# Performance work log

Hardware: AMD Instinct MI355X
Metric: run time of the kernel (lower is better)

The kernel has to match this reference:

```python
import jax, jax.numpy as jnp
import numpy as np

ROPE_DIM = 16      # RotaryEmbedding(dim=16)
MAX_FREQ = 256.0   # freqs_for='pixel'
NUM_HEADS = 16


def _axis_freqs(n):
    # pixel mode: base freqs = linspace(1, max_freq/2, dim//2) * pi, pos = linspace(-1, 1, n)
    base = jnp.linspace(1.0, MAX_FREQ / 2.0, ROPE_DIM // 2) * jnp.pi  # (8,)
    pos = jnp.linspace(-1.0, 1.0, n)                                   # (n,)
    f = pos[:, None] * base[None, :]                                   # (n, 8)
    return jnp.repeat(f, 2, axis=-1)                                   # (n, 16) interleaved pairs


def axial_freqs(T, H, W):
    ft = jnp.broadcast_to(_axis_freqs(T)[:, None, None, :], (T, H, W, ROPE_DIM))
    fh = jnp.broadcast_to(_axis_freqs(H)[None, :, None, :], (T, H, W, ROPE_DIM))
    fw = jnp.broadcast_to(_axis_freqs(W)[None, None, :, :], (T, H, W, ROPE_DIM))
    return jnp.concatenate([ft, fh, fw], axis=-1)  # (T, H, W, 48)


def rotate_half(x):
    # interleaved pairs: (..., d*2) -> rotate each (x1, x2) -> (-x2, x1)
    x = x.reshape(*x.shape[:-1], -1, 2)
    x1, x2 = x[..., 0], x[..., 1]
    return jnp.stack([-x2, x1], axis=-1).reshape(*x.shape[:-2], -1)


def apply_rope(freqs, t):
    # freqs: (T, H, W, rot_dim); t: (B, nh, T, H, W, hd); rotate first rot_dim dims
    rd = freqs.shape[-1]
    tm, tr = t[..., :rd], t[..., rd:]
    tm = tm * jnp.cos(freqs) + rotate_half(tm) * jnp.sin(freqs)
    return jnp.concatenate([tm, tr], axis=-1)


def setup_inputs() -> dict:
    key = jax.random.key(0)
    k1, k2, k3, k4 = jax.random.split(key, 4)
    B, N, C = 2, 2048, 1152
    return {
        "x": jax.random.normal(k1, (B, N, C), dtype=jnp.float32),
        "Wqkv": jax.random.normal(k2, (C, 3 * C), dtype=jnp.float32) * 0.02,
        "Wproj": jax.random.normal(k3, (C, C), dtype=jnp.float32) * 0.02,
        "bproj": jax.random.normal(k4, (C,), dtype=jnp.float32) * 0.02,
        "T": 8, "H": 16, "W": 16,
    }


def reference(x, Wqkv, Wproj, bproj, T, H, W):
    B, N, C = x.shape
    nh = NUM_HEADS
    hd = C // nh
    qkv = (x @ Wqkv).reshape(B, N, 3, nh, hd).transpose(2, 0, 3, 1, 4)  # (3, B, nh, N, hd)
    q, k, v = qkv[0], qkv[1], qkv[2]
    # tokens -> video grid
    q = q.reshape(B, nh, T, H, W, hd)
    k = k.reshape(B, nh, T, H, W, hd)
    freqs = axial_freqs(T, H, W)  # (T, H, W, 48)
    q = apply_rope(freqs, q).reshape(B, nh, N, hd)
    k = apply_rope(freqs, k).reshape(B, nh, N, hd)
    # SDPA (no mask, no dropout in eval / kv_cache=None path)
    scale = 1.0 / np.sqrt(hd)
    attn = jax.nn.softmax(jnp.einsum('bhqd,bhkd->bhqk', q, k) * scale, axis=-1)
    o = jnp.einsum('bhqk,bhkd->bhqd', attn, v)  # (B, nh, N, hd)
    o = o.transpose(0, 2, 1, 3).reshape(B, N, C)
    return o @ Wproj + bproj
```

## Files before the change

kernel.cpp:

```cpp
#include <hip/hip_runtime.h>
#include <hip/hip_bf16.h>

#define B_   2
#define N_   2048
#define C_   1152
#define NH   16
#define HD   72
#define HDP  96
#define HDV  80
#define QSTR 3584
#define KROW 104
#define VROW 72
#define KVB  64
#define KCH  832
#define TCH  1552
#define WCH  388

typedef __attribute__((ext_vector_type(8))) short bf16x8;
typedef __attribute__((ext_vector_type(4))) float f32x4;

__device__ __forceinline__ short f2bf(float f) {
  union { float fv; unsigned int u; } v; v.fv = f;
  unsigned int r = v.u + 0x7fffu + ((v.u >> 16) & 1u);
  return (short)(r >> 16);
}

__device__ __forceinline__ float bf2f(short s) {
  union { unsigned u; float f; } v; v.u = ((unsigned)(unsigned short)s) << 16;
  return v.f;
}

__device__ __forceinline__ unsigned pack_bf16(float a, float b) {
  union { __hip_bfloat162 h; unsigned u; } c;
  c.h = __float22bfloat162_rn(make_float2(a, b));
  return c.u;
}

__device__ __forceinline__ void gload_lds16(const short* g, short* l) {
  __builtin_amdgcn_global_load_lds(
      (const __attribute__((address_space(1))) unsigned int*)g,
      (__attribute__((address_space(3))) unsigned int*)l, 16, 0, 0);
}

__global__ __launch_bounds__(256) void prep(
    const float* __restrict__ x, short* __restrict__ xb,
    const float* __restrict__ Wqkv, short* __restrict__ Wt,
    const float* __restrict__ Wproj, short* __restrict__ Wpt) {
  int bid = blockIdx.x;
  if (bid < 4608) {
    const int i = bid * 256 + threadIdx.x;
    float4 v = ((const float4*)x)[i];
    short4 s;
    s.x = f2bf(v.x); s.y = f2bf(v.y); s.z = f2bf(v.z); s.w = f2bf(v.w);
    ((short4*)xb)[i] = s;
    return;
  }
  bid -= 4608;
  const float* src; short* dst; int Cc, bx, by;
  if (bid < 4032) {
    bx = bid % 112; by = bid / 112; src = Wqkv; dst = Wt; Cc = 3456;
  } else {
    bid -= 4032;
    bx = bid % 36; by = bid / 36; src = Wproj; dst = Wpt; Cc = 1152;
  }
  __shared__ float tile[32][33];
  const int c0 = bx * 32, r0 = by * 32;
  const int tx = threadIdx.x & 31, ty = threadIdx.x >> 5;
  for (int i = ty; i < 32; i += 8)
    tile[i][tx] = (c0 + tx < Cc) ? src[(long)(r0 + i) * Cc + c0 + tx] : 0.f;
  __syncthreads();
  for (int i = ty; i < 32; i += 8)
    dst[(long)(c0 + i) * 1152 + r0 + tx] = f2bf(tile[tx][i]);
}

template<bool BIAS, bool OBF>
__global__ __launch_bounds__(256, 2) void gemm_bt(
    const short* __restrict__ A, const short* __restrict__ Bt,
    void* __restrict__ Cv, const float* __restrict__ bias,
    int M, int N, int K) {
  __shared__ __align__(16) short As[2][128 * 32];
  __shared__ __align__(16) short Bs[2][128 * 32];
  const int t = threadIdx.x;
  const int lane = t & 63, wid = t >> 6;
  const int fr = lane & 15, fq = lane >> 4;

  int lin = blockIdx.y * gridDim.x + blockIdx.x;
  const int q8 = (int)(gridDim.x * gridDim.y) >> 3;
  lin = (lin & 7) * q8 + (lin >> 3);
  const int bm = lin / (int)gridDim.x;
  const int bn = lin - bm * (int)gridDim.x;

  const int wr = (wid >> 1) * 64, wc = (wid & 1) * 64;

  const int srow = t >> 2;
  const int scol = (t & 3) * 8;
  const short* Ag = A + (long)(bm * 128 + srow) * K + scol;
  const short* Bg = Bt + (long)(bn * 128 + srow) * K + scol;

  f32x4 acc[4][4] = {};

  auto STAGE = [&](int kt, int bufi) {
    gload_lds16(Ag + kt * 32,                &As[bufi][t * 8]);
    gload_lds16(Ag + kt * 32 + (long)64 * K, &As[bufi][2048 + t * 8]);
    gload_lds16(Bg + kt * 32,                &Bs[bufi][t * 8]);
    gload_lds16(Bg + kt * 32 + (long)64 * K, &Bs[bufi][2048 + t * 8]);
  };

  const int NKT = K / 32;
  STAGE(0, 0);

  for (int kt = 0; kt < NKT; ++kt) {
    const int cur = kt & 1;
    if (kt + 1 < NKT) {
      STAGE(kt + 1, cur ^ 1);
      asm volatile("s_waitcnt vmcnt(4)" ::: "memory");
    } else {
      asm volatile("s_waitcnt vmcnt(0)" ::: "memory");
    }
    __builtin_amdgcn_s_barrier();

    bf16x8 af[4], bf[4];
    #pragma unroll
    for (int i = 0; i < 4; ++i)
      af[i] = *(const bf16x8*)(&As[cur][(wr + i * 16 + fr) * 32 + fq * 8]);
    #pragma unroll
    for (int j = 0; j < 4; ++j)
      bf[j] = *(const bf16x8*)(&Bs[cur][(wc + j * 16 + fr) * 32 + fq * 8]);
    __builtin_amdgcn_s_setprio(1);
    #pragma unroll
    for (int i = 0; i < 4; ++i)
      #pragma unroll
      for (int j = 0; j < 4; ++j)
        acc[i][j] = __builtin_amdgcn_mfma_f32_16x16x32_bf16(af[i], bf[j], acc[i][j], 0, 0, 0);
    __builtin_amdgcn_s_setprio(0);
    __builtin_amdgcn_s_barrier();
  }

  #pragma unroll
  for (int i = 0; i < 4; ++i) {
    #pragma unroll
    for (int j = 0; j < 4; ++j) {
      const long row0 = (long)bm * 128 + wr + i * 16 + fq * 4;
      const int col = bn * 128 + wc + j * 16 + fr;
      const float bv = BIAS ? bias[col] : 0.f;
      #pragma unroll
      for (int r = 0; r < 4; ++r) {
        const float val = acc[i][j][r] + bv;
        if constexpr (OBF)
          ((short*)Cv)[(row0 + r) * (long)N + col] = f2bf(val);
        else
          ((float*)Cv)[(row0 + r) * (long)N + col] = val;
      }
    }
  }
}

__global__ __launch_bounds__(512, 2) void gemm_bt256(
    const short* __restrict__ A, const short* __restrict__ Bt,
    short* __restrict__ Cv, int M, int N, int K) {
  __shared__ __align__(16) short As[2][256 * 64];
  __shared__ __align__(16) short Bs[2][256 * 64];
  const int t = threadIdx.x;
  const int lane = t & 63, wid = t >> 6;
  const int fr = lane & 15, fq = lane >> 4;
  const int wm = wid >> 2, wn = wid & 3;
  const int rx = fr & 7;

  int lin = blockIdx.y * gridDim.x + blockIdx.x;
  const int q8 = (int)(gridDim.x * gridDim.y) >> 3;
  lin = (lin & 7) * q8 + (lin >> 3);
  const int bm = lin / (int)gridDim.x;
  const int bn = lin - bm * (int)gridDim.x;

  int soff[4];
  #pragma unroll
  for (int r = 0; r < 4; ++r) {
    const int p = r * 512 + t;
    const int row = p >> 3, pc = p & 7;
    soff[r] = row * K + (pc ^ (row & 7)) * 8;
  }
  const short* Ag = A + (long)bm * 256 * K;
  const short* Bg = Bt + (long)bn * 256 * K;

  f32x4 acc[8][4] = {};

  const int NKT = K / 64;
  #pragma unroll
  for (int r = 0; r < 4; ++r)
    gload_lds16(Ag + soff[r], &As[0][(r * 512 + t) * 8]);
  #pragma unroll
  for (int r = 0; r < 4; ++r)
    gload_lds16(Bg + soff[r], &Bs[0][(r * 512 + t) * 8]);

  for (int kt = 0; kt < NKT; ++kt) {
    const int cur = kt & 1;
    const bool pre = (kt + 1 < NKT);
    asm volatile("s_waitcnt vmcnt(0)" ::: "memory");
    __builtin_amdgcn_s_barrier();
    const short* Ac = &As[cur][0];
    const short* Bc = &Bs[cur][0];
    bf16x8 af[4][2], bf0[2][2], bf1[2][2];

    if (pre) {
      #pragma unroll
      for (int r = 0; r < 4; ++r)
        gload_lds16(Ag + soff[r] + (kt + 1) * 64, &As[cur ^ 1][(r * 512 + t) * 8]);
    }
    #pragma unroll
    for (int i = 0; i < 4; ++i)
      #pragma unroll
      for (int kk = 0; kk < 2; ++kk)
        af[i][kk] = *(const bf16x8*)(Ac + (wm * 128 + i * 16 + fr) * 64 + (((kk * 4 + fq) ^ rx) * 8));
    #pragma unroll
    for (int j = 0; j < 2; ++j)
      #pragma unroll
      for (int kk = 0; kk < 2; ++kk)
        bf0[j][kk] = *(const bf16x8*)(Bc + (wn * 64 + j * 16 + fr) * 64 + (((kk * 4 + fq) ^ rx) * 8));
    __builtin_amdgcn_s_setprio(1);
    #pragma unroll
    for (int i = 0; i < 4; ++i)
      #pragma unroll
      for (int j = 0; j < 2; ++j)
        #pragma unroll
        for (int kk = 0; kk < 2; ++kk)
          acc[i][j] = __builtin_amdgcn_mfma_f32_16x16x32_bf16(af[i][kk], bf0[j][kk], acc[i][j], 0, 0, 0);
    __builtin_amdgcn_s_setprio(0);

    if (pre) {
      #pragma unroll
      for (int r = 0; r < 4; ++r)
        gload_lds16(Bg + soff[r] + (kt + 1) * 64, &Bs[cur ^ 1][(r * 512 + t) * 8]);
    }
    #pragma unroll
    for (int j = 0; j < 2; ++j)
      #pragma unroll
      for (int kk = 0; kk < 2; ++kk)
        bf1[j][kk] = *(const bf16x8*)(Bc + (wn * 64 + 32 + j * 16 + fr) * 64 + (((kk * 4 + fq) ^ rx) * 8));
    __builtin_amdgcn_s_setprio(1);
    #pragma unroll
    for (int i = 0; i < 4; ++i)
      #pragma unroll
      for (int j = 0; j < 2; ++j)
        #pragma unroll
        for (int kk = 0; kk < 2; ++kk)
          acc[i][2 + j] = __builtin_amdgcn_mfma_f32_16x16x32_bf16(af[i][kk], bf1[j][kk], acc[i][2 + j], 0, 0, 0);
    __builtin_amdgcn_s_setprio(0);

    #pragma unroll
    for (int i = 0; i < 4; ++i)
      #pragma unroll
      for (int kk = 0; kk < 2; ++kk)
        af[i][kk] = *(const bf16x8*)(Ac + (wm * 128 + 64 + i * 16 + fr) * 64 + (((kk * 4 + fq) ^ rx) * 8));
    __builtin_amdgcn_s_setprio(1);
    #pragma unroll
    for (int i = 0; i < 4; ++i)
      #pragma unroll
      for (int j = 0; j < 2; ++j)
        #pragma unroll
        for (int kk = 0; kk < 2; ++kk)
          acc[4 + i][j] = __builtin_amdgcn_mfma_f32_16x16x32_bf16(af[i][kk], bf0[j][kk], acc[4 + i][j], 0, 0, 0);
    __builtin_amdgcn_s_setprio(0);

    __builtin_amdgcn_s_setprio(1);
    #pragma unroll
    for (int i = 0; i < 4; ++i)
      #pragma unroll
      for (int j = 0; j < 2; ++j)
        #pragma unroll
        for (int kk = 0; kk < 2; ++kk)
          acc[4 + i][2 + j] = __builtin_amdgcn_mfma_f32_16x16x32_bf16(af[i][kk], bf1[j][kk], acc[4 + i][2 + j], 0, 0, 0);
    __builtin_amdgcn_s_setprio(0);
  }

  #pragma unroll
  for (int mi = 0; mi < 8; ++mi) {
    #pragma unroll
    for (int j = 0; j < 4; ++j) {
      const long row0 = (long)bm * 256 + wm * 128 + (mi >> 2) * 64 + (mi & 3) * 16 + fq * 4;
      const int col = bn * 256 + wn * 64 + j * 16 + fr;
      #pragma unroll
      for (int r = 0; r < 4; ++r)
        Cv[(row0 + r) * (long)N + col] = f2bf(acc[mi][j][r]);
    }
  }
}

__global__ __launch_bounds__(256) void rope_pack(
    const short* __restrict__ QKV, short* __restrict__ Qp,
    short* __restrict__ Kp, short* __restrict__ Vt) {
  const int blk = blockIdx.x;
  const int nt = blk & 15;
  const int h = (blk >> 4) & 15;
  const int b = blk >> 8;
  const int t = threadIdx.x;
  const int n0 = nt * 128;
  const float qscale = 0.17002324f;
  const float PI = 3.14159265358979323846f;
  const long bhn = ((long)(b * NH + h)) * N_;

  for (int idx = t; idx < 128 * 48; idx += 256) {
    const int r = idx / 48;
    const int p = idx - r * 48;
    const int n = n0 + r;
    float cs = 1.f, sn = 0.f;
    if (p < 24) {
      float pos;
      if (p < 8)       pos = -1.f + (2.f / 7.f)  * (float)(n >> 8);
      else if (p < 16) pos = -1.f + (2.f / 15.f) * (float)((n >> 4) & 15);
      else             pos = -1.f + (2.f / 15.f) * (float)(n & 15);
      const float base = (1.f + (127.f / 7.f) * (float)(p & 7)) * PI;
      const float f = pos * base;
      cs = cosf(f); sn = sinf(f);
    }
    const long rowbase = ((long)(b * N_ + n)) * QSTR + h * HD + 2 * p;
    {
      float vx = 0.f, vy = 0.f;
      if (p < 36) {
        short2 v2 = *(const short2*)(QKV + rowbase);
        vx = bf2f(v2.x); vy = bf2f(v2.y);
      }
      const float o0 = vx * cs - vy * sn;
      const float o1 = vy * cs + vx * sn;
      short2 ov; ov.x = f2bf(o0 * qscale); ov.y = f2bf(o1 * qscale);
      *(short2*)(Qp + (bhn + n) * HDP + 2 * p) = ov;
    }
    {
      float vx = 0.f, vy = 0.f;
      if (p < 36) {
        short2 v2 = *(const short2*)(QKV + rowbase + C_);
        vx = bf2f(v2.x); vy = bf2f(v2.y);
      }
      const float o0 = vx * cs - vy * sn;
      const float o1 = vy * cs + vx * sn;
      short2 ov; ov.x = f2bf(o0); ov.y = f2bf(o1);
      *(short2*)(Kp + (bhn + n) * HDP + 2 * p) = ov;
    }
  }

  __shared__ short vt[128][82];
  for (int idx = t; idx < 128 * 40; idx += 256) {
    const int r = idx / 40, p = idx - r * 40;
    short2 v2; v2.x = 0; v2.y = 0;
    if (p < 36)
      v2 = *(const short2*)(QKV + ((long)(b * N_ + n0 + r)) * QSTR + 2 * C_ + h * HD + 2 * p);
    *(short2*)(&vt[r][2 * p]) = v2;
  }
  __syncthreads();
  for (int idx = t; idx < HDV * 128; idx += 256) {
    const int d = idx >> 7, nn = idx & 127;
    const int c = nn & 31;
    const int nsrc = (nn & 96) | (((c >> 2) & 1) * 16 + ((c >> 3) & 3) * 4 + (c & 3));
    Vt[(((long)(b * NH + h)) * HDV + d) * N_ + n0 + nn] = vt[nsrc][d];
  }
}

#define QKT_STEP(BUFI, S)                                                      \
  {                                                                            \
    const short* KsC_ = &KV[(BUFI)][0];                                        \
    __builtin_amdgcn_s_setprio(1);                                             \
    _Pragma("unroll")                                                          \
    for (int j = 0; j < 4; ++j) {                                              \
      _Pragma("unroll")                                                        \
      for (int kk = 0; kk < 3; ++kk) {                                         \
        bf16x8 kf = *(const bf16x8*)(KsC_ + (j * 16 + fr) * KROW + (kk * 4 + fq) * 8); \
        S[0][j] = __builtin_amdgcn_mfma_f32_16x16x32_bf16(kf, qf[0][kk], S[0][j], 0, 0, 0); \
        S[1][j] = __builtin_amdgcn_mfma_f32_16x16x32_bf16(kf, qf[1][kk], S[1][j], 0, 0, 0); \
      }                                                                        \
    }                                                                          \
    __builtin_amdgcn_s_setprio(0);                                             \
  }

#define ATTN_STEP(T, SCUR, SNEXT)                                              \
  {                                                                            \
    const int t_ = (T);                                                        \
          \
    _Pragma("unroll")                                                          \
    for (int i = 0; i < 2; ++i) {                                              \
      float psum = 0.f;                                                        \
      _Pragma("unroll")                                                        \
      for (int j = 0; j < 4; ++j)                                              \
        _Pragma("unroll")                                                      \
        for (int r = 0; r < 4; ++r) {                                          \
          const float p = __builtin_amdgcn_exp2f(SCUR[i][j][r]);               \
          SCUR[i][j][r] = p;                                                   \
          psum += p;                                                           \
        }                                                                      \
      l_[i] += psum;                                                           \
    }                                                                          \
    asm volatile("s_waitcnt vmcnt(0)" ::: "memory");                           \
    __builtin_amdgcn_s_barrier();                                              \
    if (t_ + 2 < 32) STAGE(t_ + 2, (t_ + 2) % 3);                              \
    if (t_ + 1 < 32) {                                                         \
      _Pragma("unroll")                                                        \
      for (int i = 0; i < 2; ++i)                                              \
        _Pragma("unroll")                                                      \
        for (int j = 0; j < 4; ++j)                                            \
          SNEXT[i][j] = (f32x4){0.f, 0.f, 0.f, 0.f};                           \
      QKT_STEP((t_ + 1) % 3, SNEXT);                                           \
    }                                                                          \
                    \
    const short* VsC_ = &KV[t_ % 3][KCH * 8];                                  \
    __builtin_amdgcn_s_setprio(1);                                             \
    _Pragma("unroll")                                                          \
    for (int g = 0; g < 2; ++g) {                                              \
      union { unsigned u[4]; bf16x8 v; } pf0, pf1;                             \
      pf0.u[0] = pack_bf16(SCUR[0][2 * g][0],     SCUR[0][2 * g][1]);          \
      pf0.u[1] = pack_bf16(SCUR[0][2 * g][2],     SCUR[0][2 * g][3]);          \
      pf0.u[2] = pack_bf16(SCUR[0][2 * g + 1][0], SCUR[0][2 * g + 1][1]);      \
      pf0.u[3] = pack_bf16(SCUR[0][2 * g + 1][2], SCUR[0][2 * g + 1][3]);      \
      pf1.u[0] = pack_bf16(SCUR[1][2 * g][0],     SCUR[1][2 * g][1]);          \
      pf1.u[1] = pack_bf16(SCUR[1][2 * g][2],     SCUR[1][2 * g][3]);          \
      pf1.u[2] = pack_bf16(SCUR[1][2 * g + 1][0], SCUR[1][2 * g + 1][1]);      \
      pf1.u[3] = pack_bf16(SCUR[1][2 * g + 1][2], SCUR[1][2 * g + 1][3]);      \
      _Pragma("unroll")                                                        \
      for (int jd = 0; jd < 5; ++jd) {                                         \
        bf16x8 vf = *(const bf16x8*)(VsC_ + (jd * 16 + fr) * VROW + (g * 4 + fq) * 8); \
        accO[0][jd] = __builtin_amdgcn_mfma_f32_16x16x32_bf16(pf0.v, vf, accO[0][jd], 0, 0, 0); \
        accO[1][jd] = __builtin_amdgcn_mfma_f32_16x16x32_bf16(pf1.v, vf, accO[1][jd], 0, 0, 0); \
      }                                                                        \
    }                                                                          \
    __builtin_amdgcn_s_setprio(0);                                             \
  }

__global__ __launch_bounds__(256, 2) void attn(
    const short* __restrict__ Qp, const short* __restrict__ Kp,
    const short* __restrict__ Vt, short* __restrict__ Aproj) {
  __shared__ __align__(16) short KV[3][TCH * 8];
  int blk = blockIdx.x;
  blk = (blk & 7) * 64 + (blk >> 3);
  const int qt = blk & 15;
  const int h = (blk >> 4) & 15;
  const int b = blk >> 8;
  const int t = threadIdx.x, lane = t & 63, wid = t >> 6;
  const int fr = lane & 15, fq = lane >> 4;

  const long bh = (long)(b * NH + h);
  const short* Qg = Qp + (bh * N_ + qt * 128) * HDP;
  const short* Kg = Kp + bh * N_ * HDP;
  const short* Vg = Vt + bh * HDV * N_;

  const short* sb[7];
  int sstr[7];
  #pragma unroll
  for (int it = 0; it < 7; ++it) {
    int g = wid * WCH + (it < 6 ? it * 64 + lane : 384 + lane);
    if (g >= TCH) g = TCH - 1;
    if (g < KCH) {
      const int r = g / 13, c = g - r * 13;
      sb[it] = Kg + r * HDP + (c < 12 ? c * 8 : 0);
      sstr[it] = KVB * HDP;
    } else {
      const int v = g - KCH;
      const int r = v / 9, c = v - r * 9;
      sb[it] = Vg + r * N_ + (c < 8 ? c * 8 : 0);
      sstr[it] = KVB;
    }
  }

  bf16x8 qf[2][3];
  #pragma unroll
  for (int i = 0; i < 2; ++i)
    #pragma unroll
    for (int kk = 0; kk < 3; ++kk)
      qf[i][kk] = *(const bf16x8*)(Qg + (wid * 32 + i * 16 + fr) * HDP + kk * 32 + fq * 8);

  f32x4 accO[2][5] = {};
  float l_[2] = {0.f, 0.f};

  auto STAGE = [&](int kt, int bufi) {
    short* D = &KV[bufi][0];
    #pragma unroll
    for (int it = 0; it < 6; ++it)
      gload_lds16(sb[it] + kt * sstr[it], D + (wid * WCH + it * 64 + lane) * 8);
    if (lane < 4)
      gload_lds16(sb[6] + kt * sstr[6], D + (wid * WCH + 384 + lane) * 8);
  };

  STAGE(0, 0);
  STAGE(1, 1);
  asm volatile("s_waitcnt vmcnt(7)" ::: "memory");
  __builtin_amdgcn_s_barrier();

  f32x4 sA[2][4], sB[2][4];
  #pragma unroll
  for (int i = 0; i < 2; ++i)
    #pragma unroll
    for (int j = 0; j < 4; ++j)
      sA[i][j] = (f32x4){0.f, 0.f, 0.f, 0.f};
  QKT_STEP(0, sA);

  for (int kt2 = 0; kt2 < 16; ++kt2) {
    ATTN_STEP(2 * kt2,     sA, sB);
    ATTN_STEP(2 * kt2 + 1, sB, sA);
  }

  #pragma unroll
  for (int i = 0; i < 2; ++i) {
    l_[i] += __shfl_xor(l_[i], 16);
    l_[i] += __shfl_xor(l_[i], 32);
  }
  float linv[2] = {1.f / l_[0], 1.f / l_[1]};
  #pragma unroll
  for (int i = 0; i < 2; ++i) {
    float li[4];
    #pragma unroll
    for (int r = 0; r < 4; ++r) li[r] = __shfl(linv[i], fq * 4 + r);
    #pragma unroll
    for (int r = 0; r < 4; ++r) {
      const long n = qt * 128 + wid * 32 + i * 16 + fq * 4 + r;
      #pragma unroll
      for (int jd = 0; jd < 5; ++jd) {
        const int d = jd * 16 + fr;
        if (d < HD)
          Aproj[((long)b * N_ + n) * C_ + h * HD + d] = f2bf(accO[i][jd][r] * li[r]);
      }
    }
  }
}

extern "C" void kernel_launch(void* const* d_in, const int* in_sizes, int n_in,
                              void* d_out, int out_size, void* d_ws, size_t ws_size,
                              hipStream_t stream) {
  const float* x     = (const float*)d_in[0];
  const float* Wqkv  = (const float*)d_in[1];
  const float* Wproj = (const float*)d_in[2];
  const float* bproj = (const float*)d_in[3];
  float* out = (float*)d_out;

  char* ws = (char*)d_ws;
  short* QKVb = (short*)ws;         size_t off = (size_t)4096 * QSTR * 2;
  short* xb  = (short*)(ws + off);  off += (size_t)4096 * 1152 * 2;
  short* Wt  = (short*)(ws + off);  off += (size_t)QSTR * 1152 * 2;
  short* Wpt = (short*)(ws + off);  off += (size_t)1152 * 1152 * 2;
  short* Qp  = (short*)(ws + off);  off += (size_t)B_ * NH * N_ * HDP * 2;
  short* Kp  = (short*)(ws + off);  off += (size_t)B_ * NH * N_ * HDP * 2;
  short* Vt  = (short*)(ws + off);  off += (size_t)B_ * NH * HDV * N_ * 2;
  short* Ap  = (short*)(ws + off);  off += (size_t)4096 * 1152 * 2;

  prep<<<4608 + 4032 + 1296, 256, 0, stream>>>(x, xb, Wqkv, Wt, Wproj, Wpt);
  gemm_bt256<<<dim3(QSTR / 256, 4096 / 256), 512, 0, stream>>>(
      xb, Wt, QKVb, 4096, QSTR, 1152);
  rope_pack<<<B_ * NH * (N_ / 128), 256, 0, stream>>>(QKVb, Qp, Kp, Vt);
  attn<<<B_ * NH * (N_ / 128), 256, 0, stream>>>(Qp, Kp, Vt, Ap);
  gemm_bt<true, false><<<dim3(1152 / 128, 4096 / 128), 256, 0, stream>>>(
      Ap, Wpt, (void*)out, bproj, 4096, 1152, 1152);
}
```

Measured before the change: 172.0 us.

## Split GEMM LDS tiles into halves and stage prefetch per half with fine-grained waits

Splits the A and B shared-memory tiles of the 256x256 bf16 GEMM into two 128-row halves. The next k-tile is now prefetched one half at a time, interleaved between the four MFMA phases, with a partial vmcnt wait instead of draining all loads. This aims to spread global-to-LDS traffic across the loop and shorten the stall at the top of each iteration. It adds four extra workgroup barriers per k-step, and relies on the vmcnt(2) count matching the number of outstanding loads.

```diff
diff --git a/kernel.cpp b/kernel.cpp
--- a/kernel.cpp
+++ b/kernel.cpp
@@ -158,12 +158,14 @@
 __global__ __launch_bounds__(512, 2) void gemm_bt256(
     const short* __restrict__ A, const short* __restrict__ Bt,
     short* __restrict__ Cv, int M, int N, int K) {
-  __shared__ __align__(16) short As[2][256 * 64];
-  __shared__ __align__(16) short Bs[2][256 * 64];
+  __shared__ __align__(16) short As[2][2][128 * 64];
+  __shared__ __align__(16) short Bs[2][2][128 * 64];
   const int t = threadIdx.x;
   const int lane = t & 63, wid = t >> 6;
   const int fr = lane & 15, fq = lane >> 4;
   const int wm = wid >> 2, wn = wid & 3;
+  const int bh = wn >> 1;
+  const int boff = (wn & 1) * 64;
   const int rx = fr & 7;
 
   int lin = blockIdx.y * gridDim.x + blockIdx.x;
@@ -172,50 +174,54 @@
   const int bm = lin / (int)gridDim.x;
   const int bn = lin - bm * (int)gridDim.x;
 
-  int soff[4];
-  #pragma unroll
-  for (int r = 0; r < 4; ++r) {
+  int soff[2];
+  #pragma unroll
+  for (int r = 0; r < 2; ++r) {
     const int p = r * 512 + t;
     const int row = p >> 3, pc = p & 7;
-    soff[r] = row * K + (pc ^ (row & 7)) * 8;
+    soff[r] = row * K + ((pc ^ (row & 7)) * 8);
   }
   const short* Ag = A + (long)bm * 256 * K;
   const short* Bg = Bt + (long)bn * 256 * K;
 
+  auto STG = [&](int mat, int half, int kt, int buf) {
+    const short* src = (mat ? Bg : Ag) + (long)(half * 128) * K + kt * 64;
+    short* dst = mat ? &Bs[buf][half][0] : &As[buf][half][0];
+    #pragma unroll
+    for (int r = 0; r < 2; ++r)
+      gload_lds16(src + soff[r], dst + (r * 512 + t) * 8);
+  };
+
   f32x4 acc[8][4] = {};
-
   const int NKT = K / 64;
-  #pragma unroll
-  for (int r = 0; r < 4; ++r)
-    gload_lds16(Ag + soff[r], &As[0][(r * 512 + t) * 8]);
-  #pragma unroll
-  for (int r = 0; r < 4; ++r)
-    gload_lds16(Bg + soff[r], &Bs[0][(r * 512 + t) * 8]);
+
+  STG(0, 0, 0, 0); STG(0, 1, 0, 0); STG(1, 0, 0, 0); STG(1, 1, 0, 0);
 
   for (int kt = 0; kt < NKT; ++kt) {
     const int cur = kt & 1;
     const bool pre = (kt + 1 < NKT);
-    asm volatile("s_waitcnt vmcnt(0)" ::: "memory");
-    __builtin_amdgcn_s_barrier();
-    const short* Ac = &As[cur][0];
-    const short* Bc = &Bs[cur][0];
+    const short* Ac = &As[cur][wm][0];
+    const short* Bc = &Bs[cur][bh][0];
     bf16x8 af[4][2], bf0[2][2], bf1[2][2];
 
     if (pre) {
-      #pragma unroll
-      for (int r = 0; r < 4; ++r)
-        gload_lds16(Ag + soff[r] + (kt + 1) * 64, &As[cur ^ 1][(r * 512 + t) * 8]);
-    }
+      STG(0, 0, kt + 1, cur ^ 1);
+      asm volatile("s_waitcnt vmcnt(2)" ::: "memory");
+    } else {
+      asm volatile("s_waitcnt vmcnt(0)" ::: "memory");
+    }
+    __builtin_amdgcn_s_barrier();
+
     #pragma unroll
     for (int i = 0; i < 4; ++i)
       #pragma unroll
       for (int kk = 0; kk < 2; ++kk)
-        af[i][kk] = *(const bf16x8*)(Ac + (wm * 128 + i * 16 + fr) * 64 + (((kk * 4 + fq) ^ rx) * 8));
+        af[i][kk] = *(const bf16x8*)(Ac + (i * 16 + fr) * 64 + (((kk * 4 + fq) ^ rx) * 8));
     #pragma unroll
     for (int j = 0; j < 2; ++j)
       #pragma unroll
       for (int kk = 0; kk < 2; ++kk)
-        bf0[j][kk] = *(const bf16x8*)(Bc + (wn * 64 + j * 16 + fr) * 64 + (((kk * 4 + fq) ^ rx) * 8));
+        bf0[j][kk] = *(const bf16x8*)(Bc + (boff + j * 16 + fr) * 64 + (((kk * 4 + fq) ^ rx) * 8));
     __builtin_amdgcn_s_setprio(1);
     #pragma unroll
     for (int i = 0; i < 4; ++i)
@@ -225,17 +231,14 @@
         for (int kk = 0; kk < 2; ++kk)
           acc[i][j] = __builtin_amdgcn_mfma_f32_16x16x32_bf16(af[i][kk], bf0[j][kk], acc[i][j], 0, 0, 0);
     __builtin_amdgcn_s_setprio(0);
-
-    if (pre) {
-      #pragma unroll
-      for (int r = 0; r < 4; ++r)
-        gload_lds16(Bg + soff[r] + (kt + 1) * 64, &Bs[cur ^ 1][(r * 512 + t) * 8]);
-    }
+    __builtin_amdgcn_s_barrier();
+
+    if (pre) STG(0, 1, kt + 1, cur ^ 1);
     #pragma unroll
     for (int j = 0; j < 2; ++j)
       #pragma unroll
       for (int kk = 0; kk < 2; ++kk)
-        bf1[j][kk] = *(const bf16x8*)(Bc + (wn * 64 + 32 + j * 16 + fr) * 64 + (((kk * 4 + fq) ^ rx) * 8));
+        bf1[j][kk] = *(const bf16x8*)(Bc + (boff + 32 + j * 16 + fr) * 64 + (((kk * 4 + fq) ^ rx) * 8));
     __builtin_amdgcn_s_setprio(1);
     #pragma unroll
     for (int i = 0; i < 4; ++i)
@@ -245,12 +248,14 @@
         for (int kk = 0; kk < 2; ++kk)
           acc[i][2 + j] = __builtin_amdgcn_mfma_f32_16x16x32_bf16(af[i][kk], bf1[j][kk], acc[i][2 + j], 0, 0, 0);
     __builtin_amdgcn_s_setprio(0);
-
+    __builtin_amdgcn_s_barrier();
+
+    if (pre) STG(1, 0, kt + 1, cur ^ 1);
     #pragma unroll
     for (int i = 0; i < 4; ++i)
       #pragma unroll
       for (int kk = 0; kk < 2; ++kk)
-        af[i][kk] = *(const bf16x8*)(Ac + (wm * 128 + 64 + i * 16 + fr) * 64 + (((kk * 4 + fq) ^ rx) * 8));
+        af[i][kk] = *(const bf16x8*)(Ac + (64 + i * 16 + fr) * 64 + (((kk * 4 + fq) ^ rx) * 8));
     __builtin_amdgcn_s_setprio(1);
     #pragma unroll
     for (int i = 0; i < 4; ++i)
@@ -260,7 +265,9 @@
         for (int kk = 0; kk < 2; ++kk)
           acc[4 + i][j] = __builtin_amdgcn_mfma_f32_16x16x32_bf16(af[i][kk], bf0[j][kk], acc[4 + i][j], 0, 0, 0);
     __builtin_amdgcn_s_setprio(0);
-
+    __builtin_amdgcn_s_barrier();
+
+    if (pre) STG(1, 1, kt + 1, cur ^ 1);
     __builtin_amdgcn_s_setprio(1);
     #pragma unroll
     for (int i = 0; i < 4; ++i)
@@ -270,6 +277,7 @@
         for (int kk = 0; kk < 2; ++kk)
           acc[4 + i][2 + j] = __builtin_amdgcn_mfma_f32_16x16x32_bf16(af[i][kk], bf1[j][kk], acc[4 + i][2 + j], 0, 0, 0);
     __builtin_amdgcn_s_setprio(0);
+    __builtin_amdgcn_s_barrier();
   }
 
   #pragma unroll
@@ -373,7 +381,6 @@
 #define ATTN_STEP(T, SCUR, SNEXT)                                              \
   {                                                                            \
     const int t_ = (T);                                                        \
-          \
     _Pragma("unroll")                                                          \
     for (int i = 0; i < 2; ++i) {                                              \
       float psum = 0.f;                                                        \
@@ -398,7 +405,6 @@
           SNEXT[i][j] = (f32x4){0.f, 0.f, 0.f, 0.f};                           \
       QKT_STEP((t_ + 1) % 3, SNEXT);                                           \
     }                                                                          \
-                    \
     const short* VsC_ = &KV[t_ % 3][KCH * 8];                                  \
     __builtin_amdgcn_s_setprio(1);                                             \
     _Pragma("unroll")                                                          \
```

Result: slower. 176.8 us (+2.8%).
